# Optimization experiments

Measured on AMD Instinct MI355X. Metric: run time of the kernel, lower is better.

The kernel has to match this reference:

```python
import jax, jax.numpy as jnp
import numpy as np

TAU = 1.0
EPS = 1e-5


def _gcn_sparse(x, src, dst, ew, W, b, n):
    # PyG GCNConv: add self-loops (weight 1), sym-normalize, aggregate src->dst
    deg = jax.ops.segment_sum(ew, dst, num_segments=n) + 1.0
    dinv = jnp.where(deg > 0, jax.lax.rsqrt(deg), 0.0)
    h = x @ W
    coef = dinv[src] * ew * dinv[dst]              # [E]
    out = jax.ops.segment_sum(h[src] * coef[:, None], dst, num_segments=n)
    out = out + h * (dinv * dinv)[:, None]         # self-loop term
    return out + b


def _gcn_dense(x, A, W, b):
    # x: [B,N,d], A: [B,N,N] with A[b,i,j] = weight of edge j->i
    n = A.shape[-1]
    Ah = A + jnp.eye(n, dtype=A.dtype)
    deg = Ah.sum(-1)
    dinv = jnp.where(deg > 0, jax.lax.rsqrt(deg), 0.0)
    An = dinv[:, :, None] * Ah * dinv[:, None, :]
    return jnp.einsum('bij,bjd->bid', An, x @ W) + b


def _bn_silu(x, g, be, axes):
    # BatchNorm over node axis (training-mode batch stats, biased var) + SiLU
    m = x.mean(axes, keepdims=True)
    v = x.var(axes, keepdims=True)
    return jax.nn.silu(g * (x - m) * jax.lax.rsqrt(v + EPS) + be)


def setup_inputs() -> dict:
    key = jax.random.key(0)
    ks = jax.random.split(key, 12)
    B, NPG, EPER = 32, 1024, 16384
    CIN, C, K1, K2, OUT = 64, 128, 128, 32, 10
    N, E = B * NPG, B * EPER
    ei = jax.random.randint(ks[0], (2, E), 0, NPG, dtype=jnp.int32)
    off = jnp.repeat(jnp.arange(B, dtype=jnp.int32) * NPG, EPER)
    edge_index = ei + off[None, :]
    x = jax.random.normal(ks[1], (N, CIN), jnp.float32)
    batch = jnp.repeat(jnp.arange(B, dtype=jnp.int32), NPG)
    batch_ptr = jnp.arange(B + 1, dtype=jnp.int32) * NPG
    p = lambda k, s: jax.random.normal(k, s, jnp.float32) * 0.05
    return dict(
        x=x, edge_index=edge_index, batch=batch, batch_ptr=batch_ptr,
        w1a=p(ks[2], (CIN, C)), b1a=jnp.zeros((C,)), g1a=jnp.ones((C,)), be1a=jnp.zeros((C,)),
        w1b=p(ks[3], (C, C)), b1b=jnp.zeros((C,)), g1b=jnp.ones((C,)), be1b=jnp.zeros((C,)),
        wp1=p(ks[4], (C, K1)), bp1=jnp.zeros((K1,)),
        w2a=p(ks[5], (C, C)), b2a=jnp.zeros((C,)), g2a=jnp.ones((C,)), be2a=jnp.zeros((C,)),
        w2b=p(ks[6], (C, C)), b2b=jnp.zeros((C,)), g2b=jnp.ones((C,)), be2b=jnp.zeros((C,)),
        wp2=p(ks[7], (C, K2)), bp2=jnp.zeros((K2,)),
        wl=p(ks[8], (C, OUT)), bl=jnp.zeros((OUT,)))


def reference(x, edge_index, batch, batch_ptr,
              w1a, b1a, g1a, be1a, w1b, b1b, g1b, be1b, wp1, bp1,
              w2a, b2a, g2a, be2a, w2b, b2b, g2b, be2b, wp2, bp2,
              wl, bl):
    n = x.shape[0]
    B = batch_ptr.shape[0] - 1
    npg = n // B                                    # uniform nodes per graph
    src, dst = edge_index[0], edge_index[1]
    ew = jnp.ones((edge_index.shape[1],), x.dtype)  # edge_weight=None -> ones

    # ---- stack 1: sparse GCN residual blocks + stochastic pool ----
    h = _bn_silu(_gcn_sparse(x, src, dst, ew, w1a, b1a, n), g1a, be1a, 0)
    h = h + _bn_silu(_gcn_sparse(h, src, dst, ew, w1b, b1b, n), g1b, be1b, 0)
    s = jax.nn.softmax(_gcn_sparse(h, src, dst, ew, wp1, bp1, n) / TAU, -1)  # [n,K1]
    s3 = s.reshape(B, npg, -1)
    x2 = jnp.einsum('bnc,bnd->bcd', s3, h.reshape(B, npg, -1))   # s^T x  [B,K1,C]
    t = jax.ops.segment_sum(s[src] * ew[:, None], dst, num_segments=n)  # A s
    A2 = jnp.einsum('bnc,bnk->bck', s3, t.reshape(B, npg, -1))   # s^T A s [B,K1,K1]

    # ---- stack 2: dense GCN on pooled graph + stochastic pool ----
    h2 = _bn_silu(_gcn_dense(x2, A2, w2a, b2a), g2a, be2a, (0, 1))
    h2 = h2 + _bn_silu(_gcn_dense(h2, A2, w2b, b2b), g2b, be2b, (0, 1))
    s2 = jax.nn.softmax(_gcn_dense(h2, A2, wp2, bp2) / TAU, -1)  # [B,K1,K2]
    x3 = jnp.einsum('bnc,bnd->bcd', s2, h2)                      # [B,K2,C]

    # global mean pool over nodes per graph, linear, log_softmax
    g = x3.mean(axis=1)
    out = jax.nn.log_softmax(g @ wl + bl, axis=1)
    # aux losses are multiplied by 0 in the original forward -> exact zero
    return (out, jnp.zeros((), x.dtype))
```

## Files before the change

### kernel.cpp

```cpp
#include <hip/hip_runtime.h>
#include <cmath>

#define KSPLIT 8
#define ELL_ST 80
#define NSLOT 32

typedef __attribute__((ext_vector_type(8))) short short8;
typedef __attribute__((ext_vector_type(4))) float float4v;

static __device__ __forceinline__ unsigned short f2bf(float f){
  union { float f; unsigned u; } c; c.f = f;
  unsigned r = c.u + 0x7fff + ((c.u >> 16) & 1);
  return (unsigned short)(r >> 16);
}
static __device__ __forceinline__ float u2f(unsigned u){
  union { unsigned u; float f; } c; c.u = u; return c.f;
}
static __device__ __forceinline__ float silu(float y){ return y/(1.f+__expf(-y)); }

static __device__ __forceinline__ void coef_prologue(const float* __restrict__ stats,
                                                     const float* __restrict__ gamma,
                                                     const float* __restrict__ beta,
                                                     float invM, float* lds, int tbase){
  int t = threadIdx.x - tbase;
  if(t >= 0 && t < 128){
    float s = 0.f, q = 0.f;
    #pragma unroll
    for(int k=0;k<NSLOT;k++){ s += stats[k*128+t]; q += stats[NSLOT*128 + k*128+t]; }
    float m = s*invM;
    float v = q*invM - m*m;
    float sc = gamma[t]*rsqrtf(v + 1e-5f);
    lds[t] = sc;
    lds[128+t] = beta[t] - m*sc;
  }
}

__global__ void k_fill_wt(const int* __restrict__ src, const int* __restrict__ dst,
                          int* __restrict__ cursor, int* __restrict__ esrc, int E,
                          const float* __restrict__ w1a, const float* __restrict__ w1b,
                          const float* __restrict__ wp1, const float* __restrict__ w2a,
                          const float* __restrict__ w2b,
                          unsigned short* __restrict__ t1a, unsigned short* __restrict__ t1b,
                          unsigned short* __restrict__ tp1, unsigned short* __restrict__ t2a,
                          unsigned short* __restrict__ t2b,
                          const float* __restrict__ xin, unsigned short* __restrict__ xb,
                          int NX, int CIN){
  int i = blockIdx.x*256 + threadIdx.x;
  if(i < E){
    int d = dst[i];
    int p = atomicAdd(&cursor[d], 1);
    if(p < ELL_ST) esrc[(size_t)d*ELL_ST + p] = src[i];
  } else {
    int j = i - E;
    int n1 = CIN*128, n2 = 128*128;
    if(j >= 0 && j < n1){
      int k = j >> 7, c = j & 127;
      t1a[(size_t)c*CIN + k] = f2bf(w1a[j]);
    } else if(j >= n1 && j < n1+n2){
      int jj = j - n1; int k = jj >> 7, c = jj & 127;
      t1b[(size_t)c*128 + k] = f2bf(w1b[jj]);
    } else if(j >= n1+n2 && j < n1+2*n2){
      int jj = j - n1 - n2; int k = jj >> 7, c = jj & 127;
      tp1[(size_t)c*128 + k] = f2bf(wp1[jj]);
    } else if(j >= n1+2*n2 && j < n1+3*n2){
      int jj = j - n1 - 2*n2; int k = jj >> 7, c = jj & 127;
      t2a[(size_t)c*128 + k] = f2bf(w2a[jj]);
    } else if(j >= n1+3*n2 && j < n1+4*n2){
      int jj = j - n1 - 3*n2; int k = jj >> 7, c = jj & 127;
      t2b[(size_t)c*128 + k] = f2bf(w2b[jj]);
    } else if(j >= n1+4*n2 && j < n1+4*n2+NX){
      int jj = j - n1 - 4*n2;
      xb[jj] = f2bf(xin[jj]);
    }
  }
}

template<bool ABF16>
__global__ void k_gemm_mfma(const void* __restrict__ A, const void* __restrict__ A2,
                            const unsigned short* __restrict__ Bt,
                            unsigned short* __restrict__ Cb,
                            unsigned short* __restrict__ Hout, int M, int K,
                            const int* __restrict__ rowdeg,
                            const float* __restrict__ rowscale,
                            const float* __restrict__ stA, const float* __restrict__ gA,
                            const float* __restrict__ beA,
                            const float* __restrict__ stB, const float* __restrict__ gB,
                            const float* __restrict__ beB, float invM){
  __shared__ unsigned short Abf[64][40];
  __shared__ unsigned short Bbf[128][40];
  __shared__ float lcA[256], lcB[256];
  int tid = threadIdx.x;
  if(stA) coef_prologue(stA, gA, beA, invM, lcA, 0);
  if(stB) coef_prologue(stB, gB, beB, invM, lcB, 128);
  if(stA || stB) __syncthreads();
  int wv = tid >> 6, lane = tid & 63;
  int quad = lane >> 4, l16 = lane & 15;
  int row0 = blockIdx.x*64;
  int sr = tid >> 2, sk = (tid & 3)*8;
  int srb = tid >> 1, skb = (tid & 1)*16;
  float4v acc[8] = {};
  for(int kt=0; kt<K; kt+=32){
    uint4 pk;
    if(ABF16){
      const unsigned short* ap = (const unsigned short*)A + (size_t)(row0+sr)*K + kt + sk;
      uint4 u = *(const uint4*)ap;
      if(stA){
        float va[8];
        va[0]=u2f(u.x<<16); va[1]=u2f(u.x&0xffff0000u);
        va[2]=u2f(u.y<<16); va[3]=u2f(u.y&0xffff0000u);
        va[4]=u2f(u.z<<16); va[5]=u2f(u.z&0xffff0000u);
        va[6]=u2f(u.w<<16); va[7]=u2f(u.w&0xffff0000u);
        if(stB){
          const unsigned short* bp = (const unsigned short*)A2 + (size_t)(row0+sr)*K + kt + sk;
          uint4 v = *(const uint4*)bp;
          float vb[8];
          vb[0]=u2f(v.x<<16); vb[1]=u2f(v.x&0xffff0000u);
          vb[2]=u2f(v.y<<16); vb[3]=u2f(v.y&0xffff0000u);
          vb[4]=u2f(v.z<<16); vb[5]=u2f(v.z&0xffff0000u);
          vb[6]=u2f(v.w<<16); vb[7]=u2f(v.w&0xffff0000u);
          #pragma unroll
          for(int i=0;i<8;i++){
            int c = kt+sk+i;
            va[i] = silu(lcA[c]*va[i] + lcA[128+c]) + silu(lcB[c]*vb[i] + lcB[128+c]);
          }
        } else {
          #pragma unroll
          for(int i=0;i<8;i++){
            int c = kt+sk+i;
            va[i] = silu(lcA[c]*va[i] + lcA[128+c]);
          }
        }
        pk.x = (unsigned)f2bf(va[0]) | ((unsigned)f2bf(va[1])<<16);
        pk.y = (unsigned)f2bf(va[2]) | ((unsigned)f2bf(va[3])<<16);
        pk.z = (unsigned)f2bf(va[4]) | ((unsigned)f2bf(va[5])<<16);
        pk.w = (unsigned)f2bf(va[6]) | ((unsigned)f2bf(va[7])<<16);
      } else {
        pk = u;
      }
    } else {
      const float* ap = (const float*)A + (size_t)(row0+sr)*K + kt + sk;
      float va[8];
      *(float4*)&va[0] = *(const float4*)ap;
      *(float4*)&va[4] = *(const float4*)(ap+4);
      if(stA){
        #pragma unroll
        for(int i=0;i<8;i++){
          int c = kt+sk+i;
          va[i] = silu(lcA[c]*va[i] + lcA[128+c]);
        }
      }
      pk.x = (unsigned)f2bf(va[0]) | ((unsigned)f2bf(va[1])<<16);
      pk.y = (unsigned)f2bf(va[2]) | ((unsigned)f2bf(va[3])<<16);
      pk.z = (unsigned)f2bf(va[4]) | ((unsigned)f2bf(va[5])<<16);
      pk.w = (unsigned)f2bf(va[6]) | ((unsigned)f2bf(va[7])<<16);
    }
    *(uint4*)&Abf[sr][sk] = pk;
    if(Hout)
      *(uint4*)&Hout[(size_t)(row0+sr)*128 + kt + sk] = pk;
    *(uint4*)&Bbf[srb][skb]   = *(const uint4*)&Bt[(size_t)srb*K + kt + skb];
    *(uint4*)&Bbf[srb][skb+8] = *(const uint4*)&Bt[(size_t)srb*K + kt + skb + 8];
    __syncthreads();
    short8 af = *(const short8*)&Abf[wv*16 + l16][quad*8];
    #pragma unroll
    for(int t=0;t<8;t++){
      short8 bf = *(const short8*)&Bbf[t*16 + l16][quad*8];
      acc[t] = __builtin_amdgcn_mfma_f32_16x16x32_bf16(af, bf, acc[t], 0, 0, 0);
    }
    __syncthreads();
  }
  float scr[4];
  #pragma unroll
  for(int r=0;r<4;r++){
    int grow = row0 + wv*16 + quad*4 + r;
    scr[r] = rowdeg ? rsqrtf((float)rowdeg[grow] + 1.0f) : (rowscale ? rowscale[grow] : 1.f);
  }
  #pragma unroll
  for(int t=0;t<8;t++){
    #pragma unroll
    for(int r=0;r<4;r++){
      int grow = row0 + wv*16 + quad*4 + r;
      Cb[(size_t)grow*128 + t*16 + l16] = f2bf(acc[t][r]*scr[r]);
    }
  }
}

template<bool DO_SOFTMAX, bool GCN, bool STATS, bool BF16IN, bool BF16OUT>
__global__ void k_gather(const int* __restrict__ degc, const int* __restrict__ esrc,
                         const void* __restrict__ hWs,
                         const float* __restrict__ bias, float* __restrict__ out,
                         float* __restrict__ stats){
  __shared__ float lsum[4][128];
  __shared__ float lsq[4][128];
  const unsigned short* h16 = (const unsigned short*)hWs;
  const float* h32 = (const float*)hWs;
  int wave = threadIdx.x >> 6;
  int lane = threadIdx.x & 63;
  int bid = blockIdx.x;
  int d = ((bid & 7) << 12) | ((bid >> 3) << 2) | wave;
  int grp = lane >> 5;
  int c4 = (lane & 31)*4;
  int dgr = degc[d];
  int cnt = dgr > ELL_ST ? ELL_ST : dgr;
  cnt = __builtin_amdgcn_readfirstlane(cnt);
  const int* row = esrc + (size_t)d*ELL_ST;

  auto loadrow = [&](int s)->float4{
    if(BF16IN){
      uint2 u = *(const uint2*)&h16[(size_t)s*128 + c4];
      float4 v;
      v.x = u2f(u.x << 16); v.y = u2f(u.x & 0xffff0000u);
      v.z = u2f(u.y << 16); v.w = u2f(u.y & 0xffff0000u);
      return v;
    } else {
      return *(const float4*)&h32[(size_t)s*128 + c4];
    }
  };

  float4 a0 = {0.f,0.f,0.f,0.f}, a1 = {0.f,0.f,0.f,0.f};
  float4 a2 = {0.f,0.f,0.f,0.f}, a3 = {0.f,0.f,0.f,0.f};
  if(GCN && grp == 0)
    a0 = loadrow(d);
  for(int base=0; base<cnt; base+=32){
    int m = cnt - base; if(m > 32) m = 32;
    int idx = (lane < m) ? row[base + lane] : 0;
    int full = m & ~7;
    int j0 = 0;
    for(; j0 < full; j0 += 8){
      int s0 = __shfl(idx, j0+grp);
      int s1 = __shfl(idx, j0+grp+2);
      int s2 = __shfl(idx, j0+grp+4);
      int s3 = __shfl(idx, j0+grp+6);
      float4 v0 = loadrow(s0);
      float4 v1 = loadrow(s1);
      float4 v2 = loadrow(s2);
      float4 v3 = loadrow(s3);
      a0.x+=v0.x; a0.y+=v0.y; a0.z+=v0.z; a0.w+=v0.w;
      a1.x+=v1.x; a1.y+=v1.y; a1.z+=v1.z; a1.w+=v1.w;
      a2.x+=v2.x; a2.y+=v2.y; a2.z+=v2.z; a2.w+=v2.w;
      a3.x+=v3.x; a3.y+=v3.y; a3.z+=v3.z; a3.w+=v3.w;
    }
    if(j0 < m){
      int jj0 = j0+grp, jj1 = j0+grp+2, jj2 = j0+grp+4, jj3 = j0+grp+6;
      int s0 = __shfl(idx, jj0 < m ? jj0 : 0);
      int s1 = __shfl(idx, jj1 < m ? jj1 : 0);
      int s2 = __shfl(idx, jj2 < m ? jj2 : 0);
      int s3 = __shfl(idx, jj3 < m ? jj3 : 0);
      if(jj0 < m){ float4 v = loadrow(s0);
        a0.x+=v.x; a0.y+=v.y; a0.z+=v.z; a0.w+=v.w; }
      if(jj1 < m){ float4 v = loadrow(s1);
        a1.x+=v.x; a1.y+=v.y; a1.z+=v.z; a1.w+=v.w; }
      if(jj2 < m){ float4 v = loadrow(s2);
        a2.x+=v.x; a2.y+=v.y; a2.z+=v.z; a2.w+=v.w; }
      if(jj3 < m){ float4 v = loadrow(s3);
        a3.x+=v.x; a3.y+=v.y; a3.z+=v.z; a3.w+=v.w; }
    }
  }
  float4 acc;
  acc.x = (a0.x+a1.x)+(a2.x+a3.x);
  acc.y = (a0.y+a1.y)+(a2.y+a3.y);
  acc.z = (a0.z+a1.z)+(a2.z+a3.z);
  acc.w = (a0.w+a1.w)+(a2.w+a3.w);
  acc.x += __shfl_xor(acc.x, 32);
  acc.y += __shfl_xor(acc.y, 32);
  acc.z += __shfl_xor(acc.z, 32);
  acc.w += __shfl_xor(acc.w, 32);
  float4 val = acc;
  if(GCN){
    float dv = rsqrtf((float)dgr + 1.0f);
    float4 bi = *(const float4*)&bias[c4];
    val.x = dv*acc.x + bi.x; val.y = dv*acc.y + bi.y;
    val.z = dv*acc.z + bi.z; val.w = dv*acc.w + bi.w;
  }
  if(DO_SOFTMAX){
    float mx = fmaxf(fmaxf(val.x,val.y), fmaxf(val.z,val.w));
    #pragma unroll
    for(int o=1;o<32;o<<=1) mx = fmaxf(mx, __shfl_xor(mx,o));
    float4 e; e.x=__expf(val.x-mx); e.y=__expf(val.y-mx);
    e.z=__expf(val.z-mx); e.w=__expf(val.w-mx);
    float s = e.x+e.y+e.z+e.w;
    #pragma unroll
    for(int o=1;o<32;o<<=1) s += __shfl_xor(s,o);
    float inv = 1.f/s;
    val.x=e.x*inv; val.y=e.y*inv; val.z=e.z*inv; val.w=e.w*inv;
  }
  if(grp == 0){
    if(BF16OUT){
      unsigned short* o16 = (unsigned short*)out;
      uint2 w;
      w.x = (unsigned)f2bf(val.x) | ((unsigned)f2bf(val.y)<<16);
      w.y = (unsigned)f2bf(val.z) | ((unsigned)f2bf(val.w)<<16);
      *(uint2*)&o16[(size_t)d*128 + c4] = w;
    } else {
      *(float4*)&out[(size_t)d*128 + c4] = val;
    }
  }
  if(STATS){
    if(grp == 0){
      *(float4*)&lsum[wave][c4] = val;
      float4 q; q.x=val.x*val.x; q.y=val.y*val.y; q.z=val.z*val.z; q.w=val.w*val.w;
      *(float4*)&lsq[wave][c4] = q;
    }
    __syncthreads();
    int t = threadIdx.x;
    int slot = bid & (NSLOT-1);
    if(t < 128){
      float s = (lsum[0][t]+lsum[1][t]) + (lsum[2][t]+lsum[3][t]);
      atomicAdd(&stats[slot*128 + t], s);
    } else {
      int c = t - 128;
      float q = (lsq[0][c]+lsq[1][c]) + (lsq[2][c]+lsq[3][c]);
      atomicAdd(&stats[NSLOT*128 + slot*128 + c], q);
    }
  }
}

__global__ __launch_bounds__(256, 2)
void k_pool2(const unsigned short* __restrict__ P, const unsigned short* __restrict__ QH,
             const unsigned short* __restrict__ QT,
             float* __restrict__ part1, float* __restrict__ part2, int npg, int nb){
  __shared__ unsigned short sT[128][40];
  __shared__ unsigned short qT[128][40];
  int tid = threadIdx.x;
  bool zq = (blockIdx.z == 0);
  const unsigned short* Q = zq ? QH : QT;
  int ks = blockIdx.x, b = blockIdx.y;
  int klen = npg / KSPLIT;
  size_t base = ((size_t)b*npg + (size_t)ks*klen)*128;
  int wv = tid >> 6, lane = tid & 63;
  int quad = lane >> 4, l16 = lane & 15;
  int wr = (wv >> 1)*64, wc = (wv & 1)*64;
  int arr = tid >> 7;
  int t7 = tid & 127;
  int sg = (t7 >> 4)*16;
  int sr2 = (t7 & 15)*2;
  float4v acc[4][4] = {};

  for(int c0 = 0; c0 < klen; c0 += 32){
    size_t i0 = base + (size_t)(c0+sr2)*128 + sg;
    const unsigned short* Sp = arr ? Q : P;
    unsigned short (*dstT)[40] = arr ? qT : sT;
    uint4 ua = *(const uint4*)&Sp[i0];
    uint4 ub = *(const uint4*)&Sp[i0+8];
    uint4 uc = *(const uint4*)&Sp[i0+128];
    uint4 ud = *(const uint4*)&Sp[i0+136];
    unsigned short lo[16], hi[16];
    *(uint4*)&lo[0]=ua; *(uint4*)&lo[8]=ub;
    *(uint4*)&hi[0]=uc; *(uint4*)&hi[8]=ud;
    #pragma unroll
    for(int j=0;j<16;j++)
      *(unsigned*)&dstT[sg+j][sr2] = (unsigned)lo[j] | ((unsigned)hi[j]<<16);
    __syncthreads();
    #pragma unroll
    for(int i=0;i<4;i++){
      short8 af = *(const short8*)&sT[wr + i*16 + l16][quad*8];
      #pragma unroll
      for(int j=0;j<4;j++){
        short8 bf = *(const short8*)&qT[wc + j*16 + l16][quad*8];
        acc[i][j] = __builtin_amdgcn_mfma_f32_16x16x32_bf16(af, bf, acc[i][j], 0, 0, 0);
      }
    }
    __syncthreads();
  }

  float* outp = (zq ? part1 : part2) + ((size_t)(ks*nb + b)*128)*128;
  #pragma unroll
  for(int i=0;i<4;i++)
    #pragma unroll
    for(int r=0;r<4;r++){
      int m = wr + i*16 + quad*4 + r;
      #pragma unroll
      for(int j=0;j<4;j++)
        outp[(size_t)m*128 + wc + j*16 + l16] = acc[i][j][r];
    }
}

__global__ void k_pool_reduce2(const float* __restrict__ p1, const float* __restrict__ p2,
                               float* __restrict__ x2, unsigned short* __restrict__ A2b,
                               float* __restrict__ dinv2, int total){
  int i = blockIdx.x*256 + threadIdx.x;
  int half = total >> 2;
  if(i < half){
    float4 s = *(const float4*)&p1[(size_t)i*4];
    #pragma unroll
    for(int ks=1; ks<KSPLIT; ks++){
      float4 v = *(const float4*)&p1[(size_t)ks*total + (size_t)i*4];
      s.x+=v.x; s.y+=v.y; s.z+=v.z; s.w+=v.w;
    }
    *(float4*)&x2[(size_t)i*4] = s;
  } else {
    int ia = i - half;
    float4 s = *(const float4*)&p2[(size_t)ia*4];
    #pragma unroll
    for(int ks=1; ks<KSPLIT; ks++){
      float4 v = *(const float4*)&p2[(size_t)ks*total + (size_t)ia*4];
      s.x+=v.x; s.y+=v.y; s.z+=v.z; s.w+=v.w;
    }
    uint2 w;
    w.x = (unsigned)f2bf(s.x) | ((unsigned)f2bf(s.y)<<16);
    w.y = (unsigned)f2bf(s.z) | ((unsigned)f2bf(s.w)<<16);
    *(uint2*)&A2b[(size_t)ia*4] = w;
    float rs = s.x+s.y+s.z+s.w;
    #pragma unroll
    for(int o=16;o>0;o>>=1) rs += __shfl_xor(rs, o);
    if((threadIdx.x & 31) == 0) dinv2[ia>>5] = rsqrtf(rs + 1.0f);
  }
}

template<bool ACT>
__global__ void k_dense2(const float* __restrict__ Ain,
                         const unsigned short* __restrict__ Wt,
                         const unsigned short* __restrict__ A2b,
                         const float* __restrict__ dinv2, const float* __restrict__ bias,
                         const float* __restrict__ stA, const float* __restrict__ gA,
                         const float* __restrict__ beA, float invM,
                         float* __restrict__ outp, float* __restrict__ stats){
  __shared__ unsigned short Abf[64][40];
  __shared__ unsigned short Bbf[128][40];
  __shared__ unsigned short Xt[128][136];
  __shared__ float ssum[128], ssq[128];
  __shared__ float lc[256];
  int tid = threadIdx.x;
  int b = blockIdx.x;
  if(ACT) coef_prologue(stA, gA, beA, invM, lc, 0);
  if(tid < 128){ ssum[tid] = 0.f; ssq[tid] = 0.f; }
  __syncthreads();
  int wv = tid >> 6, lane = tid & 63;
  int quad = lane >> 4, l16 = lane & 15;
  int sr = tid >> 2, sk = (tid & 3)*8;
  int srb = tid >> 1, skb = (tid & 1)*16;

  for(int half = 0; half < 2; half++){
    float4v acc[8] = {};
    for(int kt=0; kt<128; kt+=32){
      const float* ap = &Ain[((size_t)b*128 + half*64 + sr)*128 + kt + sk];
      float va[8];
      *(float4*)&va[0] = *(const float4*)ap;
      *(float4*)&va[4] = *(const float4*)(ap+4);
      if(ACT){
        #pragma unroll
        for(int i=0;i<8;i++){
          int c = kt+sk+i;
          va[i] = silu(lc[c]*va[i] + lc[128+c]);
        }
      }
      uint4 pk;
      pk.x = (unsigned)f2bf(va[0]) | ((unsigned)f2bf(va[1])<<16);
      pk.y = (unsigned)f2bf(va[2]) | ((unsigned)f2bf(va[3])<<16);
      pk.z = (unsigned)f2bf(va[4]) | ((unsigned)f2bf(va[5])<<16);
      pk.w = (unsigned)f2bf(va[6]) | ((unsigned)f2bf(va[7])<<16);
      *(uint4*)&Abf[sr][sk] = pk;
      *(uint4*)&Bbf[srb][skb]   = *(const uint4*)&Wt[(size_t)srb*128 + kt + skb];
      *(uint4*)&Bbf[srb][skb+8] = *(const uint4*)&Wt[(size_t)srb*128 + kt + skb + 8];
      __syncthreads();
      short8 af = *(const short8*)&Abf[wv*16 + l16][quad*8];
      #pragma unroll
      for(int t=0;t<8;t++){
        short8 bf = *(const short8*)&Bbf[t*16 + l16][quad*8];
        acc[t] = __builtin_amdgcn_mfma_f32_16x16x32_bf16(af, bf, acc[t], 0, 0, 0);
      }
      __syncthreads();
    }
    #pragma unroll
    for(int t=0;t<8;t++){
      #pragma unroll
      for(int r=0;r<4;r++){
        int m = half*64 + wv*16 + quad*4 + r;
        float dv = dinv2[b*128 + m];
        Xt[t*16 + l16][m] = f2bf(acc[t][r]*dv);
      }
    }
    __syncthreads();
  }

  int wr = (wv >> 1)*64, wc = (wv & 1)*64;
  float4v acc2[4][4] = {};
  for(int n0 = 0; n0 < 128; n0 += 32){
    const unsigned short* ap = &A2b[((size_t)b*128 + (tid>>1))*128 + n0 + (tid&1)*16];
    *(uint4*)&Bbf[tid>>1][(tid&1)*16]     = *(const uint4*)ap;
    *(uint4*)&Bbf[tid>>1][(tid&1)*16 + 8] = *(const uint4*)(ap + 8);
    __syncthreads();
    #pragma unroll
    for(int i=0;i<4;i++){
      short8 af = *(const short8*)&Bbf[wr + i*16 + l16][quad*8];
      #pragma unroll
      for(int j=0;j<4;j++){
        short8 bf = *(const short8*)&Xt[wc + j*16 + l16][n0 + quad*8];
        acc2[i][j] = __builtin_amdgcn_mfma_f32_16x16x32_bf16(af, bf, acc2[i][j], 0, 0, 0);
      }
    }
    __syncthreads();
  }

  float sv[4] = {}, sq[4] = {};
  #pragma unroll
  for(int i=0;i<4;i++){
    #pragma unroll
    for(int r=0;r<4;r++){
      int m = wr + i*16 + quad*4 + r;
      float dv = dinv2[b*128 + m];
      #pragma unroll
      for(int j=0;j<4;j++){
        int c = wc + j*16 + l16;
        float xr = u2f((unsigned)Xt[c][m] << 16);
        float v = dv*(acc2[i][j][r] + xr) + bias[c];
        outp[((size_t)(b*128 + m))*128 + c] = v;
        sv[j] += v; sq[j] += v*v;
      }
    }
  }
  #pragma unroll
  for(int j=0;j<4;j++){
    int c = wc + j*16 + l16;
    atomicAdd(&ssum[c], sv[j]);
    atomicAdd(&ssq[c], sq[j]);
  }
  __syncthreads();
  if(tid < 128){
    int slot = b & (NSLOT-1);
    atomicAdd(&stats[slot*128 + tid], ssum[tid]);
    atomicAdd(&stats[NSLOT*128 + slot*128 + tid], ssq[tid]);
  }
}

__global__ void k_final(const float* __restrict__ dTa, const float* __restrict__ dTb,
                        const float* __restrict__ stA, const float* __restrict__ gA,
                        const float* __restrict__ beA,
                        const float* __restrict__ stB, const float* __restrict__ gB,
                        const float* __restrict__ beB, float invMc,
                        const float* __restrict__ wl, const float* __restrict__ bl,
                        float* __restrict__ out, int K1n, int Cc, float inv_k2,
                        int OUTc, int zero_idx){
  __shared__ float lcA[256], lcB[256];
  __shared__ float red[256];
  __shared__ float gsh[128];
  __shared__ float logits[32];
  __shared__ float mred, lred;
  coef_prologue(stA, gA, beA, invMc, lcA, 0);
  coef_prologue(stB, gB, beB, invMc, lcB, 128);
  __syncthreads();
  int b = blockIdx.x;
  int tid = threadIdx.x;
  int c = tid & 127, rh = tid >> 7;
  const float* pa = dTa + (size_t)b*K1n*Cc;
  const float* pb = dTb + (size_t)b*K1n*Cc;
  float sa = lcA[c], ha = lcA[128+c], sb = lcB[c], hb = lcB[128+c];
  float acc = 0.f;
  for(int r = rh; r < K1n; r += 2){
    float ya = sa*pa[(size_t)r*Cc + c] + ha;
    float yb = sb*pb[(size_t)r*Cc + c] + hb;
    acc += silu(ya) + silu(yb);
  }
  red[tid] = acc;
  __syncthreads();
  if(tid < 128) gsh[tid] = (red[tid] + red[tid+128]) * inv_k2;
  __syncthreads();
  if(tid < OUTc){
    float l = bl[tid];
    for(int d=0; d<Cc; d++) l += gsh[d]*wl[d*OUTc + tid];
    logits[tid] = l;
  }
  __syncthreads();
  if(tid==0){
    float m = -1e30f;
    for(int o=0;o<OUTc;o++) m = fmaxf(m, logits[o]);
    float s = 0.f;
    for(int o=0;o<OUTc;o++) s += __expf(logits[o]-m);
    mred = m; lred = logf(s);
  }
  __syncthreads();
  if(tid < OUTc) out[b*OUTc + tid] = logits[tid] - mred - lred;
  if(b==0 && tid==0 && zero_idx >= 0) out[zero_idx] = 0.f;
}

extern "C" void kernel_launch(void* const* d_in, const int* in_sizes, int n_in,
                              void* d_out, int out_size, void* d_ws, size_t ws_size,
                              hipStream_t stream){
  const float* x    = (const float*)d_in[0];
  const int*   ei   = (const int*)d_in[1];
  const float* w1a  = (const float*)d_in[4];
  const float* b1a  = (const float*)d_in[5];
  const float* g1a  = (const float*)d_in[6];
  const float* be1a = (const float*)d_in[7];
  const float* w1b  = (const float*)d_in[8];
  const float* b1b  = (const float*)d_in[9];
  const float* g1b  = (const float*)d_in[10];
  const float* be1b = (const float*)d_in[11];
  const float* wp1  = (const float*)d_in[12];
  const float* bp1  = (const float*)d_in[13];
  const float* w2a  = (const float*)d_in[14];
  const float* b2a  = (const float*)d_in[15];
  const float* g2a  = (const float*)d_in[16];
  const float* be2a = (const float*)d_in[17];
  const float* w2b  = (const float*)d_in[18];
  const float* b2b  = (const float*)d_in[19];
  const float* g2b  = (const float*)d_in[20];
  const float* be2b = (const float*)d_in[21];
  const float* wl   = (const float*)d_in[24];
  const float* bl   = (const float*)d_in[25];
  float* out = (float*)d_out;

  const int C_   = in_sizes[5];
  const int CIN_ = in_sizes[4]/C_;
  const int N    = in_sizes[0]/CIN_;
  const int E    = in_sizes[1]/2;
  const int B_   = in_sizes[3]-1;
  const int NPG_ = N/B_;
  const int K1_  = in_sizes[13];
  const int K2_  = in_sizes[23];
  const int OUTc = in_sizes[25];
  const int M2   = B_*K1_;
  const int total = M2*C_;
  const int NX   = N*CIN_;

  const int* srcI = ei;
  const int* dstI = ei + E;

  float* ws = (float*)d_ws;
  size_t o = 0;
  unsigned short* bufW = (unsigned short*)(ws + o); o += (size_t)N*C_/2;
  unsigned short* bufA = (unsigned short*)(ws + o); o += (size_t)N*C_/2;
  unsigned short* bufB = (unsigned short*)(ws + o); o += (size_t)N*C_/2;
  unsigned short* bufS = (unsigned short*)(ws + o); o += (size_t)N*C_/2;
  unsigned short* bufT = (unsigned short*)(ws + o); o += (size_t)N*C_/2;
  unsigned short* bufH = (unsigned short*)(ws + o); o += (size_t)N*C_/2;
  unsigned short* xbf  = (unsigned short*)(ws + o); o += (size_t)NX/2 + 64;
  float* x2    = ws + o; o += (size_t)total;
  unsigned short* A2b = (unsigned short*)(ws + o); o += (size_t)total/2;
  float* dinv2 = ws + o; o += (size_t)M2;
  float* st1a  = ws + o; o += 2*NSLOT*128;
  float* st1b  = ws + o; o += 2*NSLOT*128;
  float* stDa  = ws + o; o += 2*NSLOT*128;
  float* stDb  = ws + o; o += 2*NSLOT*128;
  int* cursor  = (int*)(ws + o); o += (size_t)N;
  float* part  = ws + o; o += (size_t)KSPLIT*total;
  float* part2 = ws + o; o += (size_t)KSPLIT*total;
  float* dTa = part + (size_t)total;
  float* dTb = part + 2*(size_t)total;
  unsigned short* wt1a = (unsigned short*)(ws + o); o += (size_t)CIN_*C_/2 + 64;
  unsigned short* wt1b = (unsigned short*)(ws + o); o += (size_t)C_*C_/2 + 64;
  unsigned short* wtp1 = (unsigned short*)(ws + o); o += (size_t)C_*C_/2 + 64;
  unsigned short* wt2a = (unsigned short*)(ws + o); o += (size_t)C_*C_/2 + 64;
  unsigned short* wt2b = (unsigned short*)(ws + o); o += (size_t)C_*C_/2 + 64;
  int* esrc    = (int*)(ws + o); o += (size_t)N*ELL_ST;
  (void)ws_size; (void)n_in;

  dim3 blk256(256);
  auto g1 = [](int n){ return dim3((unsigned)((n+255)/256)); };
  const float invN = 1.0f/N, invM2 = 1.0f/M2;

  hipMemsetAsync(st1a, 0, (size_t)4*2*NSLOT*128*sizeof(float) + (size_t)N*sizeof(int), stream);
  k_fill_wt<<<g1(E + CIN_*C_ + 4*C_*C_ + NX), blk256, 0, stream>>>(srcI, dstI, cursor, esrc, E,
      w1a, w1b, wp1, w2a, w2b, wt1a, wt1b, wtp1, wt2a, wt2b, x, xbf, NX, CIN_);

  dim3 gath((unsigned)(N/4));
  dim3 gmm((unsigned)(N/64));

  k_gemm_mfma<true><<<gmm, blk256, 0, stream>>>(xbf, nullptr, wt1a, bufW, nullptr, N, CIN_, cursor,
      nullptr, nullptr, nullptr, nullptr, nullptr, nullptr, nullptr, 0.f);
  k_gather<false,true,true,true,true><<<gath, blk256, 0, stream>>>(cursor, esrc, bufW, b1a, (float*)bufA, st1a);

  k_gemm_mfma<true><<<gmm, blk256, 0, stream>>>(bufA, nullptr, wt1b, bufW, nullptr, N, C_, cursor,
      nullptr, st1a, g1a, be1a, nullptr, nullptr, nullptr, invN);
  k_gather<false,true,true,true,true><<<gath, blk256, 0, stream>>>(cursor, esrc, bufW, b1b, (float*)bufB, st1b);

  k_gemm_mfma<true><<<gmm, blk256, 0, stream>>>(bufA, bufB, wtp1, bufW, bufH, N, C_, cursor,
      nullptr, st1a, g1a, be1a, st1b, g1b, be1b, invN);
  k_gather<true,true,false,true,true><<<gath, blk256, 0, stream>>>(cursor, esrc, bufW, bp1, (float*)bufS, nullptr);
  k_gather<false,false,false,true,true><<<gath, blk256, 0, stream>>>(cursor, esrc, bufS, nullptr, (float*)bufT, nullptr);

  k_pool2<<<dim3(KSPLIT, B_, 2), blk256, 0, stream>>>(bufS, bufH, bufT,
      part, part2, NPG_, B_);
  k_pool_reduce2<<<g1(total/2), blk256, 0, stream>>>(part, part2, x2, A2b, dinv2, total);

  k_dense2<false><<<dim3((unsigned)B_), blk256, 0, stream>>>(x2, wt2a, A2b, dinv2, b2a,
      nullptr, nullptr, nullptr, 0.f, dTa, stDa);
  k_dense2<true><<<dim3((unsigned)B_), blk256, 0, stream>>>(dTa, wt2b, A2b, dinv2, b2b,
      stDa, g2a, be2a, invM2, dTb, stDb);

  int zero_idx = (out_size > B_*OUTc) ? B_*OUTc : -1;
  k_final<<<dim3((unsigned)B_), blk256, 0, stream>>>(dTa, dTb,
      stDa, g2a, be2a, stDb, g2b, be2b, invM2, wl, bl, out, K1_, C_, 1.0f/K2_,
      OUTc, zero_idx);
}
```

Measured before the change: 323.9 us.

## Widen gather loads to 16B per lane and swizzle dense LDS tile

The sparse gather kernel now has each lane load 8 bf16 values (16 bytes) instead of 4, with four row groups per wave and two accumulators instead of two groups and four accumulators. The reduction becomes a two-step xor shuffle and the softmax reduces over 16 lanes. The goal is fewer, wider memory transactions on the irregular row gathers, traded against less memory-level parallelism per lane. Separately, the Xt LDS tile in the dense kernel gets an XOR-style column swizzle to cut bank conflicts on the transposed writes and reads.

```diff
diff --git a/kernel.cpp b/kernel.cpp
--- a/kernel.cpp
+++ b/kernel.cpp
@@ -184,121 +184,106 @@
   }
 }
 
-template<bool DO_SOFTMAX, bool GCN, bool STATS, bool BF16IN, bool BF16OUT>
+template<bool DO_SOFTMAX, bool GCN, bool STATS, bool BF16OUT>
 __global__ void k_gather(const int* __restrict__ degc, const int* __restrict__ esrc,
-                         const void* __restrict__ hWs,
+                         const unsigned short* __restrict__ h16,
                          const float* __restrict__ bias, float* __restrict__ out,
                          float* __restrict__ stats){
   __shared__ float lsum[4][128];
   __shared__ float lsq[4][128];
-  const unsigned short* h16 = (const unsigned short*)hWs;
-  const float* h32 = (const float*)hWs;
   int wave = threadIdx.x >> 6;
   int lane = threadIdx.x & 63;
   int bid = blockIdx.x;
   int d = ((bid & 7) << 12) | ((bid >> 3) << 2) | wave;
-  int grp = lane >> 5;
-  int c4 = (lane & 31)*4;
+  int g4 = lane >> 4;
+  int c8 = (lane & 15)*8;
   int dgr = degc[d];
   int cnt = dgr > ELL_ST ? ELL_ST : dgr;
   cnt = __builtin_amdgcn_readfirstlane(cnt);
   const int* row = esrc + (size_t)d*ELL_ST;
 
-  auto loadrow = [&](int s)->float4{
-    if(BF16IN){
-      uint2 u = *(const uint2*)&h16[(size_t)s*128 + c4];
-      float4 v;
-      v.x = u2f(u.x << 16); v.y = u2f(u.x & 0xffff0000u);
-      v.z = u2f(u.y << 16); v.w = u2f(u.y & 0xffff0000u);
-      return v;
-    } else {
-      return *(const float4*)&h32[(size_t)s*128 + c4];
-    }
+  float a0[8] = {}, a1[8] = {};
+  auto addrow = [&](int s, float* a){
+    uint4 u = *(const uint4*)&h16[(size_t)s*128 + c8];
+    a[0] += u2f(u.x << 16); a[1] += u2f(u.x & 0xffff0000u);
+    a[2] += u2f(u.y << 16); a[3] += u2f(u.y & 0xffff0000u);
+    a[4] += u2f(u.z << 16); a[5] += u2f(u.z & 0xffff0000u);
+    a[6] += u2f(u.w << 16); a[7] += u2f(u.w & 0xffff0000u);
   };
-
-  float4 a0 = {0.f,0.f,0.f,0.f}, a1 = {0.f,0.f,0.f,0.f};
-  float4 a2 = {0.f,0.f,0.f,0.f}, a3 = {0.f,0.f,0.f,0.f};
-  if(GCN && grp == 0)
-    a0 = loadrow(d);
+  if(GCN && g4 == 0) addrow(d, a0);
   for(int base=0; base<cnt; base+=32){
     int m = cnt - base; if(m > 32) m = 32;
     int idx = (lane < m) ? row[base + lane] : 0;
     int full = m & ~7;
     int j0 = 0;
     for(; j0 < full; j0 += 8){
-      int s0 = __shfl(idx, j0+grp);
-      int s1 = __shfl(idx, j0+grp+2);
-      int s2 = __shfl(idx, j0+grp+4);
-      int s3 = __shfl(idx, j0+grp+6);
-      float4 v0 = loadrow(s0);
-      float4 v1 = loadrow(s1);
-      float4 v2 = loadrow(s2);
-      float4 v3 = loadrow(s3);
-      a0.x+=v0.x; a0.y+=v0.y; a0.z+=v0.z; a0.w+=v0.w;
-      a1.x+=v1.x; a1.y+=v1.y; a1.z+=v1.z; a1.w+=v1.w;
-      a2.x+=v2.x; a2.y+=v2.y; a2.z+=v2.z; a2.w+=v2.w;
-      a3.x+=v3.x; a3.y+=v3.y; a3.z+=v3.z; a3.w+=v3.w;
+      int s0 = __shfl(idx, j0+g4);
+      int s1 = __shfl(idx, j0+g4+4);
+      addrow(s0, a0);
+      addrow(s1, a1);
     }
     if(j0 < m){
-      int jj0 = j0+grp, jj1 = j0+grp+2, jj2 = j0+grp+4, jj3 = j0+grp+6;
+      int jj0 = j0+g4, jj1 = j0+g4+4;
       int s0 = __shfl(idx, jj0 < m ? jj0 : 0);
       int s1 = __shfl(idx, jj1 < m ? jj1 : 0);
-      int s2 = __shfl(idx, jj2 < m ? jj2 : 0);
-      int s3 = __shfl(idx, jj3 < m ? jj3 : 0);
-      if(jj0 < m){ float4 v = loadrow(s0);
-        a0.x+=v.x; a0.y+=v.y; a0.z+=v.z; a0.w+=v.w; }
-      if(jj1 < m){ float4 v = loadrow(s1);
-        a1.x+=v.x; a1.y+=v.y; a1.z+=v.z; a1.w+=v.w; }
-      if(jj2 < m){ float4 v = loadrow(s2);
-        a2.x+=v.x; a2.y+=v.y; a2.z+=v.z; a2.w+=v.w; }
-      if(jj3 < m){ float4 v = loadrow(s3);
-        a3.x+=v.x; a3.y+=v.y; a3.z+=v.z; a3.w+=v.w; }
-    }
-  }
-  float4 acc;
-  acc.x = (a0.x+a1.x)+(a2.x+a3.x);
-  acc.y = (a0.y+a1.y)+(a2.y+a3.y);
-  acc.z = (a0.z+a1.z)+(a2.z+a3.z);
-  acc.w = (a0.w+a1.w)+(a2.w+a3.w);
-  acc.x += __shfl_xor(acc.x, 32);
-  acc.y += __shfl_xor(acc.y, 32);
-  acc.z += __shfl_xor(acc.z, 32);
-  acc.w += __shfl_xor(acc.w, 32);
-  float4 val = acc;
+      if(jj0 < m) addrow(s0, a0);
+      if(jj1 < m) addrow(s1, a1);
+    }
+  }
+  float val[8];
+  #pragma unroll
+  for(int i=0;i<8;i++){
+    float v = a0[i] + a1[i];
+    v += __shfl_xor(v, 16);
+    v += __shfl_xor(v, 32);
+    val[i] = v;
+  }
   if(GCN){
     float dv = rsqrtf((float)dgr + 1.0f);
-    float4 bi = *(const float4*)&bias[c4];
-    val.x = dv*acc.x + bi.x; val.y = dv*acc.y + bi.y;
-    val.z = dv*acc.z + bi.z; val.w = dv*acc.w + bi.w;
+    float4 b0 = *(const float4*)&bias[c8];
+    float4 b1 = *(const float4*)&bias[c8+4];
+    float bb[8] = {b0.x,b0.y,b0.z,b0.w,b1.x,b1.y,b1.z,b1.w};
+    #pragma unroll
+    for(int i=0;i<8;i++) val[i] = dv*val[i] + bb[i];
   }
   if(DO_SOFTMAX){
-    float mx = fmaxf(fmaxf(val.x,val.y), fmaxf(val.z,val.w));
-    #pragma unroll
-    for(int o=1;o<32;o<<=1) mx = fmaxf(mx, __shfl_xor(mx,o));
-    float4 e; e.x=__expf(val.x-mx); e.y=__expf(val.y-mx);
-    e.z=__expf(val.z-mx); e.w=__expf(val.w-mx);
-    float s = e.x+e.y+e.z+e.w;
-    #pragma unroll
-    for(int o=1;o<32;o<<=1) s += __shfl_xor(s,o);
+    float mx = val[0];
+    #pragma unroll
+    for(int i=1;i<8;i++) mx = fmaxf(mx, val[i]);
+    #pragma unroll
+    for(int o=1;o<16;o<<=1) mx = fmaxf(mx, __shfl_xor(mx, o));
+    float s = 0.f;
+    #pragma unroll
+    for(int i=0;i<8;i++){ val[i] = __expf(val[i]-mx); s += val[i]; }
+    #pragma unroll
+    for(int o=1;o<16;o<<=1) s += __shfl_xor(s, o);
     float inv = 1.f/s;
-    val.x=e.x*inv; val.y=e.y*inv; val.z=e.z*inv; val.w=e.w*inv;
-  }
-  if(grp == 0){
+    #pragma unroll
+    for(int i=0;i<8;i++) val[i] *= inv;
+  }
+  if(g4 == 0){
     if(BF16OUT){
       unsigned short* o16 = (unsigned short*)out;
-      uint2 w;
-      w.x = (unsigned)f2bf(val.x) | ((unsigned)f2bf(val.y)<<16);
-      w.y = (unsigned)f2bf(val.z) | ((unsigned)f2bf(val.w)<<16);
-      *(uint2*)&o16[(size_t)d*128 + c4] = w;
+      uint4 w;
+      w.x = (unsigned)f2bf(val[0]) | ((unsigned)f2bf(val[1])<<16);
+      w.y = (unsigned)f2bf(val[2]) | ((unsigned)f2bf(val[3])<<16);
+      w.z = (unsigned)f2bf(val[4]) | ((unsigned)f2bf(val[5])<<16);
+      w.w = (unsigned)f2bf(val[6]) | ((unsigned)f2bf(val[7])<<16);
+      *(uint4*)&o16[(size_t)d*128 + c8] = w;
     } else {
-      *(float4*)&out[(size_t)d*128 + c4] = val;
+      *(float4*)&out[(size_t)d*128 + c8]     = *(float4*)&val[0];
+      *(float4*)&out[(size_t)d*128 + c8 + 4] = *(float4*)&val[4];
     }
   }
   if(STATS){
-    if(grp == 0){
-      *(float4*)&lsum[wave][c4] = val;
-      float4 q; q.x=val.x*val.x; q.y=val.y*val.y; q.z=val.z*val.z; q.w=val.w*val.w;
-      *(float4*)&lsq[wave][c4] = q;
+    if(g4 == 0){
+      *(float4*)&lsum[wave][c8]   = *(float4*)&val[0];
+      *(float4*)&lsum[wave][c8+4] = *(float4*)&val[4];
+      float q[8];
+      #pragma unroll
+      for(int i=0;i<8;i++) q[i] = val[i]*val[i];
+      *(float4*)&lsq[wave][c8]   = *(float4*)&q[0];
+      *(float4*)&lsq[wave][c8+4] = *(float4*)&q[4];
     }
     __syncthreads();
     int t = threadIdx.x;
@@ -465,8 +450,10 @@
       #pragma unroll
       for(int r=0;r<4;r++){
         int m = half*64 + wv*16 + quad*4 + r;
+        int cc = t*16 + l16;
         float dv = dinv2[b*128 + m];
-        Xt[t*16 + l16][m] = f2bf(acc[t][r]*dv);
+        int pm = ((((m>>3) + 2*(cc&3)) & 15) << 3) | (m & 7);
+        Xt[cc][pm] = f2bf(acc[t][r]*dv);
       }
     }
     __syncthreads();
@@ -484,7 +471,9 @@
       short8 af = *(const short8*)&Bbf[wr + i*16 + l16][quad*8];
       #pragma unroll
       for(int j=0;j<4;j++){
-        short8 bf = *(const short8*)&Xt[wc + j*16 + l16][n0 + quad*8];
+        int cc = wc + j*16 + l16;
+        int pcm = ((n0>>3) + quad + 2*(cc&3)) & 15;
+        short8 bf = *(const short8*)&Xt[cc][pcm<<3];
         acc2[i][j] = __builtin_amdgcn_mfma_f32_16x16x32_bf16(af, bf, acc2[i][j], 0, 0, 0);
       }
     }
@@ -501,7 +490,8 @@
       #pragma unroll
       for(int j=0;j<4;j++){
         int c = wc + j*16 + l16;
-        float xr = u2f((unsigned)Xt[c][m] << 16);
+        int pm = ((((m>>3) + 2*(c&3)) & 15) << 3) | (m & 7);
+        float xr = u2f((unsigned)Xt[c][pm] << 16);
         float v = dv*(acc2[i][j][r] + xr) + bias[c];
         outp[((size_t)(b*128 + m))*128 + c] = v;
         sv[j] += v; sq[j] += v*v;
@@ -556,7 +546,7 @@
   __syncthreads();
   if(tid < OUTc){
     float l = bl[tid];
-    for(int d=0; d<Cc; d++) l += gsh[d]*wl[d*OUTc + tid];
+    for(int d2=0; d2<Cc; d2++) l += gsh[d2]*wl[d2*OUTc + tid];
     logits[tid] = l;
   }
   __syncthreads();
@@ -657,16 +647,16 @@
 
   k_gemm_mfma<true><<<gmm, blk256, 0, stream>>>(xbf, nullptr, wt1a, bufW, nullptr, N, CIN_, cursor,
       nullptr, nullptr, nullptr, nullptr, nullptr, nullptr, nullptr, 0.f);
-  k_gather<false,true,true,true,true><<<gath, blk256, 0, stream>>>(cursor, esrc, bufW, b1a, (float*)bufA, st1a);
+  k_gather<false,true,true,true><<<gath, blk256, 0, stream>>>(cursor, esrc, bufW, b1a, (float*)bufA, st1a);
 
   k_gemm_mfma<true><<<gmm, blk256, 0, stream>>>(bufA, nullptr, wt1b, bufW, nullptr, N, C_, cursor,
       nullptr, st1a, g1a, be1a, nullptr, nullptr, nullptr, invN);
-  k_gather<false,true,true,true,true><<<gath, blk256, 0, stream>>>(cursor, esrc, bufW, b1b, (float*)bufB, st1b);
+  k_gather<false,true,true,true><<<gath, blk256, 0, stream>>>(cursor, esrc, bufW, b1b, (float*)bufB, st1b);
 
   k_gemm_mfma<true><<<gmm, blk256, 0, stream>>>(bufA, bufB, wtp1, bufW, bufH, N, C_, cursor,
       nullptr, st1a, g1a, be1a, st1b, g1b, be1b, invN);
-  k_gather<true,true,false,true,true><<<gath, blk256, 0, stream>>>(cursor, esrc, bufW, bp1, (float*)bufS, nullptr);
-  k_gather<false,false,false,true,true><<<gath, blk256, 0, stream>>>(cursor, esrc, bufS, nullptr, (float*)bufT, nullptr);
+  k_gather<true,true,false,true><<<gath, blk256, 0, stream>>>(cursor, esrc, bufW, bp1, (float*)bufS, nullptr);
+  k_gather<false,false,false,true><<<gath, blk256, 0, stream>>>(cursor, esrc, bufS, nullptr, (float*)bufT, nullptr);
 
   k_pool2<<<dim3(KSPLIT, B_, 2), blk256, 0, stream>>>(bufS, bufH, bufT,
       part, part2, NPG_, B_);
```

Result: no change. 328.7 us (+1.5%).

## Split dense GCN kernel across four column-quarter blocks per graph

Applied to the files above, without the earlier changes.

The dense pooled-graph GCN kernel now launches 4 blocks per graph, each computing a 32-column slice of X·W and then A·(XW) for that slice, instead of one block doing all 128 columns. This raises the grid from 32 to 128 blocks to fill more compute units. The cost is that each block re-reads and re-activates the full input rows and the A2 tile. A swizzled layout for the transposed intermediate is added to avoid LDS bank conflicts. Also removes the unused fp32 gather path template parameter.

```diff
diff --git a/kernel.cpp b/kernel.cpp
--- a/kernel.cpp
+++ b/kernel.cpp
@@ -184,15 +184,13 @@
   }
 }
 
-template<bool DO_SOFTMAX, bool GCN, bool STATS, bool BF16IN, bool BF16OUT>
+template<bool DO_SOFTMAX, bool GCN, bool STATS, bool BF16OUT>
 __global__ void k_gather(const int* __restrict__ degc, const int* __restrict__ esrc,
-                         const void* __restrict__ hWs,
+                         const unsigned short* __restrict__ h16,
                          const float* __restrict__ bias, float* __restrict__ out,
                          float* __restrict__ stats){
   __shared__ float lsum[4][128];
   __shared__ float lsq[4][128];
-  const unsigned short* h16 = (const unsigned short*)hWs;
-  const float* h32 = (const float*)hWs;
   int wave = threadIdx.x >> 6;
   int lane = threadIdx.x & 63;
   int bid = blockIdx.x;
@@ -205,15 +203,11 @@
   const int* row = esrc + (size_t)d*ELL_ST;
 
   auto loadrow = [&](int s)->float4{
-    if(BF16IN){
-      uint2 u = *(const uint2*)&h16[(size_t)s*128 + c4];
-      float4 v;
-      v.x = u2f(u.x << 16); v.y = u2f(u.x & 0xffff0000u);
-      v.z = u2f(u.y << 16); v.w = u2f(u.y & 0xffff0000u);
-      return v;
-    } else {
-      return *(const float4*)&h32[(size_t)s*128 + c4];
-    }
+    uint2 u = *(const uint2*)&h16[(size_t)s*128 + c4];
+    float4 v;
+    v.x = u2f(u.x << 16); v.y = u2f(u.x & 0xffff0000u);
+    v.z = u2f(u.y << 16); v.w = u2f(u.y & 0xffff0000u);
+    return v;
   };
 
   float4 a0 = {0.f,0.f,0.f,0.f}, a1 = {0.f,0.f,0.f,0.f};
@@ -414,111 +408,126 @@
                          const float* __restrict__ stA, const float* __restrict__ gA,
                          const float* __restrict__ beA, float invM,
                          float* __restrict__ outp, float* __restrict__ stats){
-  __shared__ unsigned short Abf[64][40];
-  __shared__ unsigned short Bbf[128][40];
-  __shared__ unsigned short Xt[128][136];
-  __shared__ float ssum[128], ssq[128];
+  __shared__ unsigned short Abf[128][40];
+  __shared__ unsigned short Bbf[32][40];
+  __shared__ unsigned short Xt[32][136];
+  __shared__ float ssum[32], ssq[32];
   __shared__ float lc[256];
   int tid = threadIdx.x;
-  int b = blockIdx.x;
+  int cq = blockIdx.x, b = blockIdx.y;
   if(ACT) coef_prologue(stA, gA, beA, invM, lc, 0);
-  if(tid < 128){ ssum[tid] = 0.f; ssq[tid] = 0.f; }
+  if(tid < 32){ ssum[tid] = 0.f; ssq[tid] = 0.f; }
   __syncthreads();
   int wv = tid >> 6, lane = tid & 63;
   int quad = lane >> 4, l16 = lane & 15;
-  int sr = tid >> 2, sk = (tid & 3)*8;
-  int srb = tid >> 1, skb = (tid & 1)*16;
-
-  for(int half = 0; half < 2; half++){
-    float4v acc[8] = {};
-    for(int kt=0; kt<128; kt+=32){
-      const float* ap = &Ain[((size_t)b*128 + half*64 + sr)*128 + kt + sk];
-      float va[8];
-      *(float4*)&va[0] = *(const float4*)ap;
-      *(float4*)&va[4] = *(const float4*)(ap+4);
-      if(ACT){
-        #pragma unroll
-        for(int i=0;i<8;i++){
-          int c = kt+sk+i;
-          va[i] = silu(lc[c]*va[i] + lc[128+c]);
-        }
-      }
-      uint4 pk;
-      pk.x = (unsigned)f2bf(va[0]) | ((unsigned)f2bf(va[1])<<16);
-      pk.y = (unsigned)f2bf(va[2]) | ((unsigned)f2bf(va[3])<<16);
-      pk.z = (unsigned)f2bf(va[4]) | ((unsigned)f2bf(va[5])<<16);
-      pk.w = (unsigned)f2bf(va[6]) | ((unsigned)f2bf(va[7])<<16);
-      *(uint4*)&Abf[sr][sk] = pk;
-      *(uint4*)&Bbf[srb][skb]   = *(const uint4*)&Wt[(size_t)srb*128 + kt + skb];
-      *(uint4*)&Bbf[srb][skb+8] = *(const uint4*)&Wt[(size_t)srb*128 + kt + skb + 8];
-      __syncthreads();
-      short8 af = *(const short8*)&Abf[wv*16 + l16][quad*8];
+
+  float4v acc[2][2] = {};
+  int ar = tid >> 1, ak = (tid & 1)*16;
+  int wr_ = tid >> 2, wk = (tid & 3)*8;
+  for(int kt=0; kt<128; kt+=32){
+    const float* ap = &Ain[((size_t)b*128 + ar)*128 + kt + ak];
+    float va[16];
+    *(float4*)&va[0]  = *(const float4*)ap;
+    *(float4*)&va[4]  = *(const float4*)(ap+4);
+    *(float4*)&va[8]  = *(const float4*)(ap+8);
+    *(float4*)&va[12] = *(const float4*)(ap+12);
+    if(ACT){
       #pragma unroll
-      for(int t=0;t<8;t++){
-        short8 bf = *(const short8*)&Bbf[t*16 + l16][quad*8];
-        acc[t] = __builtin_amdgcn_mfma_f32_16x16x32_bf16(af, bf, acc[t], 0, 0, 0);
-      }
-      __syncthreads();
-    }
-    #pragma unroll
-    for(int t=0;t<8;t++){
+      for(int i=0;i<16;i++){
+        int c = kt+ak+i;
+        va[i] = silu(lc[c]*va[i] + lc[128+c]);
+      }
+    }
+    uint4 p0, p1;
+    p0.x = (unsigned)f2bf(va[0])  | ((unsigned)f2bf(va[1])<<16);
+    p0.y = (unsigned)f2bf(va[2])  | ((unsigned)f2bf(va[3])<<16);
+    p0.z = (unsigned)f2bf(va[4])  | ((unsigned)f2bf(va[5])<<16);
+    p0.w = (unsigned)f2bf(va[6])  | ((unsigned)f2bf(va[7])<<16);
+    p1.x = (unsigned)f2bf(va[8])  | ((unsigned)f2bf(va[9])<<16);
+    p1.y = (unsigned)f2bf(va[10]) | ((unsigned)f2bf(va[11])<<16);
+    p1.z = (unsigned)f2bf(va[12]) | ((unsigned)f2bf(va[13])<<16);
+    p1.w = (unsigned)f2bf(va[14]) | ((unsigned)f2bf(va[15])<<16);
+    *(uint4*)&Abf[ar][ak]   = p0;
+    *(uint4*)&Abf[ar][ak+8] = p1;
+    if(tid < 128)
+      *(uint4*)&Bbf[wr_][wk] = *(const uint4*)&Wt[(size_t)(cq*32 + wr_)*128 + kt + wk];
+    __syncthreads();
+    #pragma unroll
+    for(int i=0;i<2;i++){
+      short8 af = *(const short8*)&Abf[wv*32 + i*16 + l16][quad*8];
       #pragma unroll
-      for(int r=0;r<4;r++){
-        int m = half*64 + wv*16 + quad*4 + r;
-        float dv = dinv2[b*128 + m];
-        Xt[t*16 + l16][m] = f2bf(acc[t][r]*dv);
-      }
-    }
-    __syncthreads();
-  }
-
-  int wr = (wv >> 1)*64, wc = (wv & 1)*64;
-  float4v acc2[4][4] = {};
-  for(int n0 = 0; n0 < 128; n0 += 32){
-    const unsigned short* ap = &A2b[((size_t)b*128 + (tid>>1))*128 + n0 + (tid&1)*16];
-    *(uint4*)&Bbf[tid>>1][(tid&1)*16]     = *(const uint4*)ap;
-    *(uint4*)&Bbf[tid>>1][(tid&1)*16 + 8] = *(const uint4*)(ap + 8);
-    __syncthreads();
-    #pragma unroll
-    for(int i=0;i<4;i++){
-      short8 af = *(const short8*)&Bbf[wr + i*16 + l16][quad*8];
-      #pragma unroll
-      for(int j=0;j<4;j++){
-        short8 bf = *(const short8*)&Xt[wc + j*16 + l16][n0 + quad*8];
-        acc2[i][j] = __builtin_amdgcn_mfma_f32_16x16x32_bf16(af, bf, acc2[i][j], 0, 0, 0);
-      }
-    }
-    __syncthreads();
-  }
-
-  float sv[4] = {}, sq[4] = {};
+      for(int j=0;j<2;j++){
+        short8 bf = *(const short8*)&Bbf[j*16 + l16][quad*8];
+        acc[i][j] = __builtin_amdgcn_mfma_f32_16x16x32_bf16(af, bf, acc[i][j], 0, 0, 0);
+      }
+    }
+    __syncthreads();
+  }
   #pragma unroll
-  for(int i=0;i<4;i++){
+  for(int i=0;i<2;i++){
     #pragma unroll
     for(int r=0;r<4;r++){
-      int m = wr + i*16 + quad*4 + r;
+      int m = wv*32 + i*16 + quad*4 + r;
       float dv = dinv2[b*128 + m];
       #pragma unroll
-      for(int j=0;j<4;j++){
-        int c = wc + j*16 + l16;
-        float xr = u2f((unsigned)Xt[c][m] << 16);
-        float v = dv*(acc2[i][j][r] + xr) + bias[c];
-        outp[((size_t)(b*128 + m))*128 + c] = v;
+      for(int j=0;j<2;j++){
+        int cc = j*16 + l16;
+        int pm = ((((m>>3) + 2*(cc&3)) & 15) << 3) | (m & 7);
+        Xt[cc][pm] = f2bf(acc[i][j][r]*dv);
+      }
+    }
+  }
+  __syncthreads();
+
+  float4v acc2[2][2] = {};
+  for(int n0 = 0; n0 < 128; n0 += 32){
+    const unsigned short* a2p = &A2b[((size_t)b*128 + (tid>>1))*128 + n0 + (tid&1)*16];
+    *(uint4*)&Abf[tid>>1][(tid&1)*16]     = *(const uint4*)a2p;
+    *(uint4*)&Abf[tid>>1][(tid&1)*16 + 8] = *(const uint4*)(a2p + 8);
+    __syncthreads();
+    #pragma unroll
+    for(int i=0;i<2;i++){
+      short8 af = *(const short8*)&Abf[wv*32 + i*16 + l16][quad*8];
+      #pragma unroll
+      for(int j=0;j<2;j++){
+        int cc = j*16 + l16;
+        int pcm = ((n0>>3) + quad + 2*(cc&3)) & 15;
+        short8 bf = *(const short8*)&Xt[cc][pcm<<3];
+        acc2[i][j] = __builtin_amdgcn_mfma_f32_16x16x32_bf16(af, bf, acc2[i][j], 0, 0, 0);
+      }
+    }
+    __syncthreads();
+  }
+
+  float sv[2] = {}, sq[2] = {};
+  #pragma unroll
+  for(int i=0;i<2;i++){
+    #pragma unroll
+    for(int r=0;r<4;r++){
+      int m = wv*32 + i*16 + quad*4 + r;
+      float dv = dinv2[b*128 + m];
+      #pragma unroll
+      for(int j=0;j<2;j++){
+        int cc = j*16 + l16;
+        int pm = ((((m>>3) + 2*(cc&3)) & 15) << 3) | (m & 7);
+        float xr = u2f((unsigned)Xt[cc][pm] << 16);
+        float v = dv*(acc2[i][j][r] + xr) + bias[cq*32 + cc];
+        outp[((size_t)(b*128 + m))*128 + cq*32 + cc] = v;
         sv[j] += v; sq[j] += v*v;
       }
     }
   }
   #pragma unroll
-  for(int j=0;j<4;j++){
-    int c = wc + j*16 + l16;
-    atomicAdd(&ssum[c], sv[j]);
-    atomicAdd(&ssq[c], sq[j]);
-  }
-  __syncthreads();
-  if(tid < 128){
+  for(int j=0;j<2;j++){
+    int cc = j*16 + l16;
+    atomicAdd(&ssum[cc], sv[j]);
+    atomicAdd(&ssq[cc], sq[j]);
+  }
+  __syncthreads();
+  if(tid < 32){
     int slot = b & (NSLOT-1);
-    atomicAdd(&stats[slot*128 + tid], ssum[tid]);
-    atomicAdd(&stats[NSLOT*128 + slot*128 + tid], ssq[tid]);
+    atomicAdd(&stats[slot*128 + cq*32 + tid], ssum[tid]);
+    atomicAdd(&stats[NSLOT*128 + slot*128 + cq*32 + tid], ssq[tid]);
   }
 }
 
@@ -556,7 +565,7 @@
   __syncthreads();
   if(tid < OUTc){
     float l = bl[tid];
-    for(int d=0; d<Cc; d++) l += gsh[d]*wl[d*OUTc + tid];
+    for(int d2=0; d2<Cc; d2++) l += gsh[d2]*wl[d2*OUTc + tid];
     logits[tid] = l;
   }
   __syncthreads();
@@ -657,24 +666,24 @@
 
   k_gemm_mfma<true><<<gmm, blk256, 0, stream>>>(xbf, nullptr, wt1a, bufW, nullptr, N, CIN_, cursor,
       nullptr, nullptr, nullptr, nullptr, nullptr, nullptr, nullptr, 0.f);
-  k_gather<false,true,true,true,true><<<gath, blk256, 0, stream>>>(cursor, esrc, bufW, b1a, (float*)bufA, st1a);
+  k_gather<false,true,true,true><<<gath, blk256, 0, stream>>>(cursor, esrc, bufW, b1a, (float*)bufA, st1a);
 
   k_gemm_mfma<true><<<gmm, blk256, 0, stream>>>(bufA, nullptr, wt1b, bufW, nullptr, N, C_, cursor,
       nullptr, st1a, g1a, be1a, nullptr, nullptr, nullptr, invN);
-  k_gather<false,true,true,true,true><<<gath, blk256, 0, stream>>>(cursor, esrc, bufW, b1b, (float*)bufB, st1b);
+  k_gather<false,true,true,true><<<gath, blk256, 0, stream>>>(cursor, esrc, bufW, b1b, (float*)bufB, st1b);
 
   k_gemm_mfma<true><<<gmm, blk256, 0, stream>>>(bufA, bufB, wtp1, bufW, bufH, N, C_, cursor,
       nullptr, st1a, g1a, be1a, st1b, g1b, be1b, invN);
-  k_gather<true,true,false,true,true><<<gath, blk256, 0, stream>>>(cursor, esrc, bufW, bp1, (float*)bufS, nullptr);
-  k_gather<false,false,false,true,true><<<gath, blk256, 0, stream>>>(cursor, esrc, bufS, nullptr, (float*)bufT, nullptr);
+  k_gather<true,true,false,true><<<gath, blk256, 0, stream>>>(cursor, esrc, bufW, bp1, (float*)bufS, nullptr);
+  k_gather<false,false,false,true><<<gath, blk256, 0, stream>>>(cursor, esrc, bufS, nullptr, (float*)bufT, nullptr);
 
   k_pool2<<<dim3(KSPLIT, B_, 2), blk256, 0, stream>>>(bufS, bufH, bufT,
       part, part2, NPG_, B_);
   k_pool_reduce2<<<g1(total/2), blk256, 0, stream>>>(part, part2, x2, A2b, dinv2, total);
 
-  k_dense2<false><<<dim3((unsigned)B_), blk256, 0, stream>>>(x2, wt2a, A2b, dinv2, b2a,
+  k_dense2<false><<<dim3(4, (unsigned)B_), blk256, 0, stream>>>(x2, wt2a, A2b, dinv2, b2a,
       nullptr, nullptr, nullptr, 0.f, dTa, stDa);
-  k_dense2<true><<<dim3((unsigned)B_), blk256, 0, stream>>>(dTa, wt2b, A2b, dinv2, b2b,
+  k_dense2<true><<<dim3(4, (unsigned)B_), blk256, 0, stream>>>(dTa, wt2b, A2b, dinv2, b2b,
       stDa, g2a, be2a, invM2, dTb, stDb);
 
   int zero_idx = (out_size > B_*OUTc) ? B_*OUTc : -1;
```

After: 316.0 us, median of 2. 1.02x faster.
